# Optimization experiments

Measured on AMD Instinct MI355X. Metric: run time of the kernel, lower is better.

The kernel has to match this reference:

```python
import jax, jax.numpy as jnp
import numpy as np

N = 50000      # nodes
E = 800000     # edges (avg degree 16)
IN = 128       # in_size
OUT = 64       # out_size
H = 32         # hidden_size
WIDTH = 3      # width
SCALE = 0.05


def _laplacian(x, src, tgt, n):
    # normalized Laplacian action: out[t] = sum_{edges into t} (x[t] - x[s]) / deg(t)
    deg = jax.ops.segment_sum(jnp.ones((tgt.shape[0],), x.dtype), tgt, num_segments=n)
    fac = 1.0 / deg[tgt]                       # [E], deg>=1 for any target that appears
    msg = (x[tgt] - x[src]) * fac[:, None]     # [E, F]
    return jax.ops.segment_sum(msg, tgt, num_segments=n)


def _grouped_linear(x, Wg, bg):
    # Conv1d(kernel=1, groups=width) == per-group linear
    n = x.shape[0]
    xg = x.reshape(n, WIDTH, -1)               # [N, width, h_in]
    out = jnp.einsum('nwh,who->nwo', xg, Wg) + bg
    return out.reshape(n, -1)                  # [N, width*h_out]


def setup_inputs() -> dict:
    key = jax.random.key(0)
    ks = jax.random.split(key, 14)
    data = jax.random.normal(ks[0], (N, IN), jnp.float32)
    src = jax.random.randint(ks[1], (E,), 0, N)
    tgt = jnp.sort(jax.random.randint(ks[2], (E,), 0, N))
    # preprocess ConvSkip: Linear(in, hidden*width) + Linear(in, hidden*width)
    W_pre = jax.random.normal(ks[3], (IN, H * WIDTH), jnp.float32) * SCALE
    b_pre = jnp.zeros((H * WIDTH,), jnp.float32)
    T_pre = jax.random.normal(ks[4], (IN, H * WIDTH), jnp.float32) * SCALE
    bT_pre = jnp.zeros((H * WIDTH,), jnp.float32)
    # middle WideConvSkip (depth-2 = 1 block): grouped conv [width, H, H]
    W_blk = jax.random.normal(ks[5], (WIDTH, H, H), jnp.float32) * SCALE
    b_blk = jnp.zeros((WIDTH, H), jnp.float32)
    T_blk = jax.random.normal(ks[6], (IN, H * WIDTH), jnp.float32) * SCALE
    bT_blk = jnp.zeros((H * WIDTH,), jnp.float32)
    # postprocess WideConvSkip: grouped conv [width, H, OUT]
    W_post = jax.random.normal(ks[7], (WIDTH, H, OUT), jnp.float32) * SCALE
    b_post = jnp.zeros((WIDTH, OUT), jnp.float32)
    T_post = jax.random.normal(ks[8], (IN, OUT * WIDTH), jnp.float32) * SCALE
    bT_post = jnp.zeros((OUT * WIDTH,), jnp.float32)
    return {"data": data, "src": src, "tgt": tgt,
            "W_pre": W_pre, "b_pre": b_pre, "T_pre": T_pre, "bT_pre": bT_pre,
            "W_blk": W_blk, "b_blk": b_blk, "T_blk": T_blk, "bT_blk": bT_blk,
            "W_post": W_post, "b_post": b_post, "T_post": T_post, "bT_post": bT_post}


def reference(data, src, tgt, W_pre, b_pre, T_pre, bT_pre,
              W_blk, b_blk, T_blk, bT_blk,
              W_post, b_post, T_post, bT_post):
    n = data.shape[0]
    # preprocess ConvSkip: sigma(L f(x) + g(x))
    out = data @ W_pre + b_pre
    out = _laplacian(out, src, tgt, n)
    out = jax.nn.relu(out + data @ T_pre + bT_pre)       # [N, H*width]
    # middle WideConvSkip (depth - 2 = 1)
    h = _grouped_linear(out, W_blk, b_blk)
    h = _laplacian(h, src, tgt, n)
    out = jax.nn.relu(h + data @ T_blk + bT_blk)          # [N, H*width]
    # postprocess WideConvSkip
    h = _grouped_linear(out, W_post, b_post)
    h = _laplacian(h, src, tgt, n)
    out = jax.nn.relu(h + data @ T_post + bT_post)        # [N, OUT*width]
    # reshape(N, -1, width) then adaptive_avg_pool1d(., 1) == mean over width
    out = out.reshape(n, -1, WIDTH)
    return out.mean(axis=-1, keepdims=True)               # [N, OUT, 1]
```

## Files before the change

### kernel.cpp

```cpp
#include <hip/hip_runtime.h>
#include <cstdint>
#include <cstddef>

#define N_NODES 50000
#define E_EDGES 800000
#define IN_F    128
#define PCOLS   512

typedef unsigned short ushortT;
typedef unsigned int   uintT;
typedef __attribute__((ext_vector_type(8))) short s8v;
typedef __attribute__((ext_vector_type(4))) float f4v;
typedef __attribute__((ext_vector_type(2))) float f2v;

__device__ __forceinline__ float bflo(uintT u){ union{uintT i;float f;}c; c.i=u<<16; return c.f; }
__device__ __forceinline__ float bfhi(uintT u){ union{uintT i;float f;}c; c.i=u&0xFFFF0000u; return c.f; }
__device__ __forceinline__ ushortT f2bfu(float f){
    union{float f;uintT u;}c; c.f=f;
    uintT r = c.u + 0x7FFF + ((c.u>>16)&1);
    return (ushortT)(r>>16);
}
__device__ __forceinline__ uintT pack2(float a, float b){
    return (uintT)f2bfu(a) | ((uintT)f2bfu(b) << 16);
}

__global__ void prep1(const float* __restrict__ A,
                      const float* __restrict__ Wp,  const float* __restrict__ bp,
                      const float* __restrict__ Tp,  const float* __restrict__ bTp,
                      const float* __restrict__ Tb,  const float* __restrict__ bTb,
                      const float* __restrict__ Tpo, const float* __restrict__ bTpo,
                      const float* __restrict__ Wpost,
                      const int* __restrict__ tgt,
                      ushortT* __restrict__ Wb, float* __restrict__ bcat,
                      float2* __restrict__ Wp2,
                      ushortT* __restrict__ Ab, int* __restrict__ row_ptr)
{
    int gid = blockIdx.x * 256 + threadIdx.x;
    {
        size_t off = (size_t)gid * 8;
        float4 v0 = *(const float4*)(A + off);
        float4 v1 = *(const float4*)(A + off + 4);
        uint4 u;
        u.x = pack2(v0.x, v0.y); u.y = pack2(v0.z, v0.w);
        u.z = pack2(v1.x, v1.y); u.w = pack2(v1.z, v1.w);
        *(uint4*)(Ab + off) = u;
    }
    if (gid < IN_F * PCOLS) {
        int k = gid >> 9;
        int c = gid & 511;
        float v;
        if      (c < 96)  v = Wp [k*96  + c];
        else if (c < 192) v = Tp [k*96  + (c-96)];
        else if (c < 288) v = Tb [k*96  + (c-192)];
        else if (c < 480) v = Tpo[k*192 + (c-288)];
        else              v = 0.f;
        Wb[(size_t)c*IN_F + k] = f2bfu(v);
        if (k == 0) {
            float b;
            if      (c < 96)  b = bp  [c];
            else if (c < 192) b = bTp [c-96];
            else if (c < 288) b = bTb [c-192];
            else if (c < 480) b = bTpo[c-288];
            else              b = 0.f;
            bcat[c] = b;
        }
        if (gid < 3*16*64) {
            int w = gid >> 10, r = gid & 1023;
            int i2 = r >> 6, j = r & 63;
            Wp2[gid] = make_float2(Wpost[(w*32 + 2*i2)*64 + j],
                                   Wpost[(w*32 + 2*i2 + 1)*64 + j]);
        }
    }
    if (gid <= N_NODES) {
        int lo = 0, hi = E_EDGES;
        while (lo < hi) {
            int mid = (lo + hi) >> 1;
            if (tgt[mid] < gid) lo = mid + 1; else hi = mid;
        }
        row_ptr[gid] = lo;
    }
}

__global__ void build_srcp(const int* __restrict__ src, const int* __restrict__ row_ptr,
                           int* __restrict__ srcp,
                           ushortT* __restrict__ Y0b, ushortT* __restrict__ rb1,
                           ushortT* __restrict__ rb2)
{
    int gid = blockIdx.x * 256 + threadIdx.x;
    int t = gid >> 6, slot = gid & 63;
    int lo = row_ptr[t];
    int deg = row_ptr[t+1] - lo;
    int v = slot < deg ? src[lo + slot] : N_NODES;
    srcp[gid] = v * 192;
    if (gid < 96) {
        Y0b[(size_t)N_NODES*96 + gid] = 0;
        rb1[(size_t)N_NODES*96 + gid] = 0;
        rb2[(size_t)N_NODES*96 + gid] = 0;
    }
}

__global__ __launch_bounds__(256, 2) void gemm_mfma(const ushortT* __restrict__ Ab,
                                                    const ushortT* __restrict__ Wb,
                                                    const float* __restrict__ bcat,
                                                    float* __restrict__ P,
                                                    ushortT* __restrict__ Y0b, int M)
{
    __shared__ ushortT Asl[128][72];
    __shared__ ushortT Bsl[128][72];
    int tid = threadIdx.x;
    int nb = blockIdx.x * 128;
    int mb = blockIdx.y * 128;
    int wv = tid >> 6, lane = tid & 63;
    int wm = wv >> 1, wn = wv & 1;
    int cl = lane & 15, q = lane >> 4;

    f4v acc[4][4];
    #pragma unroll
    for (int i = 0; i < 4; ++i)
        #pragma unroll
        for (int j = 0; j < 4; ++j) acc[i][j] = (f4v)0.f;

    for (int kt = 0; kt < IN_F; kt += 64) {
        if (kt) __syncthreads();
        #pragma unroll
        for (int r = 0; r < 4; ++r) {
            int idx = tid + 256*r;
            int row = idx >> 3, qq = idx & 7;
            int gm = mb + row;
            uint4 v = make_uint4(0,0,0,0);
            if (gm < M) v = *(const uint4*)(Ab + (size_t)gm*IN_F + kt + qq*8);
            *(uint4*)(&Asl[row][qq*8]) = v;
        }
        #pragma unroll
        for (int r = 0; r < 4; ++r) {
            int idx = tid + 256*r;
            int row = idx >> 3, qq = idx & 7;
            uint4 v = *(const uint4*)(Wb + (size_t)(nb+row)*IN_F + kt + qq*8);
            *(uint4*)(&Bsl[row][qq*8]) = v;
        }
        __syncthreads();
        #pragma unroll
        for (int ks = 0; ks < 2; ++ks) {
            int ko = ks*32 + q*8;
            s8v af[4], bf[4];
            #pragma unroll
            for (int mt = 0; mt < 4; ++mt)
                af[mt] = *(const s8v*)(&Asl[wm*64 + mt*16 + cl][ko]);
            #pragma unroll
            for (int nt = 0; nt < 4; ++nt)
                bf[nt] = *(const s8v*)(&Bsl[wn*64 + nt*16 + cl][ko]);
            #pragma unroll
            for (int mt = 0; mt < 4; ++mt)
                #pragma unroll
                for (int nt = 0; nt < 4; ++nt)
                    acc[mt][nt] = __builtin_amdgcn_mfma_f32_16x16x32_bf16(af[mt], bf[nt], acc[mt][nt], 0, 0, 0);
        }
    }

    bool y0blk = (nb == 0) && (wn == 0);
    #pragma unroll
    for (int nt = 0; nt < 4; ++nt) {
        int gn = nb + wn*64 + nt*16 + cl;
        float bv = bcat[gn];
        bool doY = y0blk && (gn < 96);
        #pragma unroll
        for (int mt = 0; mt < 4; ++mt) {
            int gm0 = mb + wm*64 + mt*16 + q*4;
            #pragma unroll
            for (int r = 0; r < 4; ++r) {
                int gm = gm0 + r;
                if (gm < M) {
                    float val = acc[mt][nt][r] + bv;
                    P[(size_t)gm*PCOLS + gn] = val;
                    if (doY) Y0b[(size_t)gm*96 + gn] = f2bfu(val);
                }
            }
        }
    }
}

#define GATHER96(Xb, lo, deg, sv, pL, sx, sy)                                     \
    float sx, sy;                                                                 \
    {                                                                             \
        f2v c0={0.f,0.f}, c1={0.f,0.f}, c2={0.f,0.f}, c3={0.f,0.f};               \
        int dmax = deg < 64 ? deg : 64;                                           \
        _Pragma("unroll 1")                                                       \
        for (int w_ = 0; w_ < dmax; w_ += 16) {                                   \
            uintT u[16];                                                          \
            _Pragma("unroll")                                                     \
            for (int kk = 0; kk < 16; ++kk) {                                     \
                int off = __builtin_amdgcn_readlane(sv, w_ + kk);                 \
                const char* rp = (const char*)(Xb) + off;                         \
                u[kk] = *(const uintT*)(rp + 4*pL);                               \
            }                                                                     \
            _Pragma("unroll")                                                     \
            for (int kk = 0; kk < 16; ++kk) {                                     \
                f2v v_; v_.x = bflo(u[kk]); v_.y = bfhi(u[kk]);                   \
                switch (kk & 3) {                                                 \
                    case 0: c0 += v_; break;                                      \
                    case 1: c1 += v_; break;                                      \
                    case 2: c2 += v_; break;                                      \
                    default:c3 += v_; break;                                      \
                }                                                                 \
            }                                                                     \
        }                                                                         \
        if (deg > 64) {                                                           \
            _Pragma("unroll 1")                                                   \
            for (int j_ = lo + 64; j_ < lo + deg; ++j_) {                         \
                int off = src[j_] * 192;                                          \
                const char* rp = (const char*)(Xb) + off;                         \
                uintT u0 = *(const uintT*)(rp + 4*pL);                            \
                f2v v_; v_.x = bflo(u0); v_.y = bfhi(u0);                         \
                c0 += v_;                                                         \
            }                                                                     \
        }                                                                         \
        f2v cs_ = (c0 + c1) + (c2 + c3);                                          \
        sx = cs_.x; sy = cs_.y;                                                   \
    }

__global__ __launch_bounds__(256) void lap1(
    const ushortT* __restrict__ Xb,
    const float*   __restrict__ Pown,
    const float*   __restrict__ Z,
    const int* __restrict__ srcp, const int* __restrict__ src,
    const int* __restrict__ row_ptr,
    ushortT* __restrict__ rb1)
{
    int lane = threadIdx.x & 63;
    int t  = __builtin_amdgcn_readfirstlane((blockIdx.x << 2) + (threadIdx.x >> 6));
    int lo = __builtin_amdgcn_readfirstlane(row_ptr[t]);
    int deg = __builtin_amdgcn_readfirstlane(row_ptr[t+1]) - lo;
    int pL = lane < 48 ? lane : 0;
    int sv = srcp[t*64 + lane];
    float2 xr = *(const float2*)(Pown + (size_t)t*PCOLS + 2*pL);
    float2 zr = *(const float2*)(Z    + (size_t)t*PCOLS + 2*pL);

    GATHER96(Xb, lo, deg, sv, pL, sx, sy)

    float inv = deg > 0 ? 1.f/(float)deg : 0.f;
    float mf  = deg > 0 ? 1.f : 0.f;
    if (lane < 48) {
        float ox = fmaxf(mf*xr.x - sx*inv + zr.x, 0.f);
        float oy = fmaxf(mf*xr.y - sy*inv + zr.y, 0.f);
        *(uintT*)(rb1 + (size_t)t*96 + 2*pL) = pack2(ox, oy);
    }
}

__global__ __launch_bounds__(256) void lap2(
    const ushortT* __restrict__ Xb,
    const float*   __restrict__ Z,
    const int* __restrict__ srcp, const int* __restrict__ src,
    const int* __restrict__ row_ptr,
    const float* __restrict__ Wblk,
    ushortT* __restrict__ rb2)
{
    __shared__ float wS[3*32*32];
    int lane = threadIdx.x & 63;
    int t  = __builtin_amdgcn_readfirstlane((blockIdx.x << 2) + (threadIdx.x >> 6));
    int pL = lane < 48 ? lane : 0;
    int sv = srcp[t*64 + lane];
    int lo = __builtin_amdgcn_readfirstlane(row_ptr[t]);
    int deg = __builtin_amdgcn_readfirstlane(row_ptr[t+1]) - lo;
    uintT ux = *(const uintT*)(Xb + (size_t)t*96 + 2*pL);
    float2 zr = *(const float2*)(Z + (size_t)t*PCOLS + 2*pL);

    for (int i = threadIdx.x; i < 3072; i += 256) wS[i] = Wblk[i];
    __syncthreads();

    int w  = pL >> 4;
    int jj = pL & 15;
    const float2* wc = ((const float2*)wS) + (w*512 + jj);

    GATHER96(Xb, lo, deg, sv, pL, sx, sy)

    float inv = deg > 0 ? 1.f/(float)deg : 0.f;
    float mf  = deg > 0 ? 1.f : 0.f;
    float Lx = mf*bflo(ux) - sx*inv;
    float Ly = mf*bfhi(ux) - sy*inv;

    float accx = 0.f, accy = 0.f;
    #pragma unroll
    for (int d = 0; d < 16; ++d) {
        int sl = w*16 + d;
        float ax = __shfl(Lx, sl);
        float ay = __shfl(Ly, sl);
        float2 wa = wc[(2*d)*16];
        float2 wb = wc[(2*d+1)*16];
        accx = fmaf(ax, wa.x, accx); accx = fmaf(ay, wb.x, accx);
        accy = fmaf(ax, wa.y, accy); accy = fmaf(ay, wb.y, accy);
    }
    if (lane < 48) {
        float ox = fmaxf(accx + zr.x, 0.f);
        float oy = fmaxf(accy + zr.y, 0.f);
        *(uintT*)(rb2 + (size_t)t*96 + 2*pL) = pack2(ox, oy);
    }
}

__global__ __launch_bounds__(256) void lap3(
    const ushortT* __restrict__ Xb,
    const float*   __restrict__ Z,
    const int* __restrict__ srcp, const int* __restrict__ src,
    const int* __restrict__ row_ptr,
    const float2* __restrict__ Wp2,
    float* __restrict__ out)
{
    __shared__ float2 wS[3*16*64];
    __shared__ float  sm[4][96];
    int lane = threadIdx.x & 63;
    int wvw  = threadIdx.x >> 6;
    int t  = __builtin_amdgcn_readfirstlane((blockIdx.x << 2) + wvw);
    int pL = lane < 48 ? lane : 0;
    int sv = srcp[t*64 + lane];
    int lo = __builtin_amdgcn_readfirstlane(row_ptr[t]);
    int deg = __builtin_amdgcn_readfirstlane(row_ptr[t+1]) - lo;
    uintT ux = *(const uintT*)(Xb + (size_t)t*96 + 2*pL);
    float z0 = Z[(size_t)t*PCOLS + lane];
    float z1 = Z[(size_t)t*PCOLS + 64 + lane];
    float z2 = Z[(size_t)t*PCOLS + 128 + lane];

    for (int i = threadIdx.x; i < 3072; i += 256) wS[i] = Wp2[i];
    __syncthreads();

    const float2* wl = wS + lane;

    GATHER96(Xb, lo, deg, sv, pL, sx, sy)

    float inv = deg > 0 ? 1.f/(float)deg : 0.f;
    float mf  = deg > 0 ? 1.f : 0.f;
    float Lx = mf*bflo(ux) - sx*inv;
    float Ly = mf*bfhi(ux) - sy*inv;

    if (lane < 48) {
        sm[wvw][2*pL]     = Lx;
        sm[wvw][2*pL + 1] = Ly;
    }
    __builtin_amdgcn_wave_barrier();

    float a0 = 0.f, a1 = 0.f, a2 = 0.f;
    #pragma unroll
    for (int w2 = 0; w2 < 3; ++w2) {
        float acc = 0.f;
        #pragma unroll
        for (int i2 = 0; i2 < 16; ++i2) {
            float2 iv = *(const float2*)(&sm[wvw][w2*32 + 2*i2]);
            float2 p  = wl[(w2*16 + i2)*64];
            acc = fmaf(iv.x, p.x, acc);
            acc = fmaf(iv.y, p.y, acc);
        }
        if (w2 == 0) a0 = acc; else if (w2 == 1) a1 = acc; else a2 = acc;
    }
    float o0 = fmaxf(a0 + z0, 0.f);
    float o1 = fmaxf(a1 + z1, 0.f);
    float o2 = fmaxf(a2 + z2, 0.f);
    float r = 0.f;
    #pragma unroll
    for (int q = 0; q < 3; ++q) {
        int c = 3*lane + q;
        int sl = c & 63, wsel = c >> 6;
        float v0 = __shfl(o0, sl);
        float v1 = __shfl(o1, sl);
        float v2 = __shfl(o2, sl);
        r += (wsel == 0) ? v0 : ((wsel == 1) ? v1 : v2);
    }
    out[(size_t)t*64 + lane] = r * (1.0f/3.0f);
}

extern "C" void kernel_launch(void* const* d_in, const int* in_sizes, int n_in,
                              void* d_out, int out_size, void* d_ws, size_t ws_size,
                              hipStream_t stream)
{
    const float* data    = (const float*)d_in[0];
    const int*   src     = (const int*)  d_in[1];
    const int*   tgt     = (const int*)  d_in[2];
    const float* W_pre   = (const float*)d_in[3];
    const float* b_pre   = (const float*)d_in[4];
    const float* T_pre   = (const float*)d_in[5];
    const float* bT_pre  = (const float*)d_in[6];
    const float* W_blk   = (const float*)d_in[7];
    const float* b_blk   = (const float*)d_in[8];
    const float* T_blk   = (const float*)d_in[9];
    const float* bT_blk  = (const float*)d_in[10];
    const float* W_post  = (const float*)d_in[11];
    const float* b_post  = (const float*)d_in[12];
    const float* T_post  = (const float*)d_in[13];
    const float* bT_post = (const float*)d_in[14];
    float* out = (float*)d_out;

    float* ws = (float*)d_ws;
    float*   P       = ws;
    float*   bcat    = P + (size_t)N_NODES * PCOLS;
    float2*  Wp2     = (float2*)(bcat + 512);
    int*     row_ptr = (int*)(Wp2 + 3*16*64);
    int*     srcp    = row_ptr + 50008;
    ushortT* Y0b     = (ushortT*)(srcp + (size_t)N_NODES*64);
    ushortT* rb1     = Y0b + (size_t)(N_NODES+1) * 96;
    ushortT* rb2     = rb1 + (size_t)(N_NODES+1) * 96;
    ushortT* Ab      = rb2 + (size_t)(N_NODES+1) * 96;
    ushortT* Wb      = Ab  + (size_t)N_NODES * IN_F;

    prep1<<<(N_NODES*IN_F/8)/256, 256, 0, stream>>>(
        data, W_pre, b_pre, T_pre, bT_pre, T_blk, bT_blk, T_post, bT_post,
        W_post, tgt, Wb, bcat, Wp2, Ab, row_ptr);

    build_srcp<<<(N_NODES*64)/256, 256, 0, stream>>>(src, row_ptr, srcp, Y0b, rb1, rb2);

    dim3 gg(PCOLS/128, (N_NODES + 127)/128);
    gemm_mfma<<<gg, 256, 0, stream>>>(Ab, Wb, bcat, P, Y0b, N_NODES);

    lap1<<<N_NODES/4, 256, 0, stream>>>(Y0b, P, P + 96, srcp, src, row_ptr, rb1);
    lap2<<<N_NODES/4, 256, 0, stream>>>(rb1, P + 192, srcp, src, row_ptr, W_blk, rb2);
    lap3<<<N_NODES/4, 256, 0, stream>>>(rb2, P + 288, srcp, src, row_ptr, Wp2, out);
}
```

Before: 303.5 us.

## Store GEMM output in bf16, drop srcp precompute, loop nodes per block

The GEMM now writes its whole 512-column output as bf16 instead of fp32 plus a separate bf16 copy, roughly halving that write traffic and the later reads of the skip terms. The build_srcp kernel is removed; each Laplacian kernel loads its neighbour indices straight from src and scales them by the row stride, with the zero padding row moved into prep1. lap2 and lap3 now process four nodes per wave so each block stages its weights in shared memory once for sixteen nodes instead of four. The cost is bf16 rounding of the skip and Laplacian inputs, and the first layer gathers from rows with a wider 512-column stride.

```diff
diff --git a/kernel.cpp b/kernel.cpp
--- a/kernel.cpp
+++ b/kernel.cpp
@@ -33,7 +33,9 @@
                       const int* __restrict__ tgt,
                       ushortT* __restrict__ Wb, float* __restrict__ bcat,
                       float2* __restrict__ Wp2,
-                      ushortT* __restrict__ Ab, int* __restrict__ row_ptr)
+                      ushortT* __restrict__ Ab, int* __restrict__ row_ptr,
+                      ushortT* __restrict__ Pb, ushortT* __restrict__ rb1,
+                      ushortT* __restrict__ rb2)
 {
     int gid = blockIdx.x * 256 + threadIdx.x;
     {
@@ -71,6 +73,11 @@
                                    Wpost[(w*32 + 2*i2 + 1)*64 + j]);
         }
     }
+    if (gid < 96) {
+        Pb [(size_t)N_NODES*PCOLS + gid] = 0;
+        rb1[(size_t)N_NODES*96   + gid] = 0;
+        rb2[(size_t)N_NODES*96   + gid] = 0;
+    }
     if (gid <= N_NODES) {
         int lo = 0, hi = E_EDGES;
         while (lo < hi) {
@@ -81,29 +88,10 @@
     }
 }
 
-__global__ void build_srcp(const int* __restrict__ src, const int* __restrict__ row_ptr,
-                           int* __restrict__ srcp,
-                           ushortT* __restrict__ Y0b, ushortT* __restrict__ rb1,
-                           ushortT* __restrict__ rb2)
-{
-    int gid = blockIdx.x * 256 + threadIdx.x;
-    int t = gid >> 6, slot = gid & 63;
-    int lo = row_ptr[t];
-    int deg = row_ptr[t+1] - lo;
-    int v = slot < deg ? src[lo + slot] : N_NODES;
-    srcp[gid] = v * 192;
-    if (gid < 96) {
-        Y0b[(size_t)N_NODES*96 + gid] = 0;
-        rb1[(size_t)N_NODES*96 + gid] = 0;
-        rb2[(size_t)N_NODES*96 + gid] = 0;
-    }
-}
-
 __global__ __launch_bounds__(256, 2) void gemm_mfma(const ushortT* __restrict__ Ab,
                                                     const ushortT* __restrict__ Wb,
                                                     const float* __restrict__ bcat,
-                                                    float* __restrict__ P,
-                                                    ushortT* __restrict__ Y0b, int M)
+                                                    ushortT* __restrict__ Pb, int M)
 {
     __shared__ ushortT Asl[128][72];
     __shared__ ushortT Bsl[128][72];
@@ -157,29 +145,23 @@
         }
     }
 
-    bool y0blk = (nb == 0) && (wn == 0);
     #pragma unroll
     for (int nt = 0; nt < 4; ++nt) {
         int gn = nb + wn*64 + nt*16 + cl;
         float bv = bcat[gn];
-        bool doY = y0blk && (gn < 96);
         #pragma unroll
         for (int mt = 0; mt < 4; ++mt) {
             int gm0 = mb + wm*64 + mt*16 + q*4;
             #pragma unroll
             for (int r = 0; r < 4; ++r) {
                 int gm = gm0 + r;
-                if (gm < M) {
-                    float val = acc[mt][nt][r] + bv;
-                    P[(size_t)gm*PCOLS + gn] = val;
-                    if (doY) Y0b[(size_t)gm*96 + gn] = f2bfu(val);
-                }
+                if (gm < M) Pb[(size_t)gm*PCOLS + gn] = f2bfu(acc[mt][nt][r] + bv);
             }
         }
     }
 }
 
-#define GATHER96(Xb, lo, deg, sv, pL, sx, sy)                                     \
+#define GATHER96(Xb, lo, deg, sv, pL, STRB, sx, sy)                               \
     float sx, sy;                                                                 \
     {                                                                             \
         f2v c0={0.f,0.f}, c1={0.f,0.f}, c2={0.f,0.f}, c3={0.f,0.f};               \
@@ -207,7 +189,7 @@
         if (deg > 64) {                                                           \
             _Pragma("unroll 1")                                                   \
             for (int j_ = lo + 64; j_ < lo + deg; ++j_) {                         \
-                int off = src[j_] * 192;                                          \
+                int off = src[j_] * (STRB);                                       \
                 const char* rp = (const char*)(Xb) + off;                         \
                 uintT u0 = *(const uintT*)(rp + 4*pL);                            \
                 f2v v_; v_.x = bflo(u0); v_.y = bfhi(u0);                         \
@@ -218,12 +200,18 @@
         sx = cs_.x; sy = cs_.y;                                                   \
     }
 
+#define MAKE_SV(lo, deg, lane, STRB, sv)                                          \
+    int sv;                                                                       \
+    {                                                                             \
+        int e_ = (lo) + (lane);                                                   \
+        if (e_ > E_EDGES - 1) e_ = E_EDGES - 1;                                   \
+        int sn_ = src[e_];                                                        \
+        sv = ((lane) < (deg) ? sn_ : N_NODES) * (STRB);                           \
+    }
+
 __global__ __launch_bounds__(256) void lap1(
-    const ushortT* __restrict__ Xb,
-    const float*   __restrict__ Pown,
-    const float*   __restrict__ Z,
-    const int* __restrict__ srcp, const int* __restrict__ src,
-    const int* __restrict__ row_ptr,
+    const ushortT* __restrict__ Pb,
+    const int* __restrict__ src, const int* __restrict__ row_ptr,
     ushortT* __restrict__ rb1)
 {
     int lane = threadIdx.x & 63;
@@ -231,138 +219,145 @@
     int lo = __builtin_amdgcn_readfirstlane(row_ptr[t]);
     int deg = __builtin_amdgcn_readfirstlane(row_ptr[t+1]) - lo;
     int pL = lane < 48 ? lane : 0;
-    int sv = srcp[t*64 + lane];
-    float2 xr = *(const float2*)(Pown + (size_t)t*PCOLS + 2*pL);
-    float2 zr = *(const float2*)(Z    + (size_t)t*PCOLS + 2*pL);
-
-    GATHER96(Xb, lo, deg, sv, pL, sx, sy)
+    MAKE_SV(lo, deg, lane, 2*PCOLS, sv)
+    uintT ux = *(const uintT*)(Pb + (size_t)t*PCOLS + 2*pL);
+    uintT zu = *(const uintT*)(Pb + (size_t)t*PCOLS + 96 + 2*pL);
+
+    GATHER96(Pb, lo, deg, sv, pL, 2*PCOLS, sx, sy)
 
     float inv = deg > 0 ? 1.f/(float)deg : 0.f;
     float mf  = deg > 0 ? 1.f : 0.f;
     if (lane < 48) {
-        float ox = fmaxf(mf*xr.x - sx*inv + zr.x, 0.f);
-        float oy = fmaxf(mf*xr.y - sy*inv + zr.y, 0.f);
+        float ox = fmaxf(mf*bflo(ux) - sx*inv + bflo(zu), 0.f);
+        float oy = fmaxf(mf*bfhi(ux) - sy*inv + bfhi(zu), 0.f);
         *(uintT*)(rb1 + (size_t)t*96 + 2*pL) = pack2(ox, oy);
     }
 }
 
 __global__ __launch_bounds__(256) void lap2(
     const ushortT* __restrict__ Xb,
-    const float*   __restrict__ Z,
-    const int* __restrict__ srcp, const int* __restrict__ src,
-    const int* __restrict__ row_ptr,
+    const ushortT* __restrict__ Pb,
+    const int* __restrict__ src, const int* __restrict__ row_ptr,
     const float* __restrict__ Wblk,
     ushortT* __restrict__ rb2)
 {
     __shared__ float wS[3*32*32];
-    int lane = threadIdx.x & 63;
-    int t  = __builtin_amdgcn_readfirstlane((blockIdx.x << 2) + (threadIdx.x >> 6));
-    int pL = lane < 48 ? lane : 0;
-    int sv = srcp[t*64 + lane];
-    int lo = __builtin_amdgcn_readfirstlane(row_ptr[t]);
-    int deg = __builtin_amdgcn_readfirstlane(row_ptr[t+1]) - lo;
-    uintT ux = *(const uintT*)(Xb + (size_t)t*96 + 2*pL);
-    float2 zr = *(const float2*)(Z + (size_t)t*PCOLS + 2*pL);
-
     for (int i = threadIdx.x; i < 3072; i += 256) wS[i] = Wblk[i];
     __syncthreads();
 
+    int lane = threadIdx.x & 63;
+    int wvw  = threadIdx.x >> 6;
+    int pL = lane < 48 ? lane : 0;
     int w  = pL >> 4;
     int jj = pL & 15;
     const float2* wc = ((const float2*)wS) + (w*512 + jj);
 
-    GATHER96(Xb, lo, deg, sv, pL, sx, sy)
-
-    float inv = deg > 0 ? 1.f/(float)deg : 0.f;
-    float mf  = deg > 0 ? 1.f : 0.f;
-    float Lx = mf*bflo(ux) - sx*inv;
-    float Ly = mf*bfhi(ux) - sy*inv;
-
-    float accx = 0.f, accy = 0.f;
-    #pragma unroll
-    for (int d = 0; d < 16; ++d) {
-        int sl = w*16 + d;
-        float ax = __shfl(Lx, sl);
-        float ay = __shfl(Ly, sl);
-        float2 wa = wc[(2*d)*16];
-        float2 wb = wc[(2*d+1)*16];
-        accx = fmaf(ax, wa.x, accx); accx = fmaf(ay, wb.x, accx);
-        accy = fmaf(ax, wa.y, accy); accy = fmaf(ay, wb.y, accy);
-    }
-    if (lane < 48) {
-        float ox = fmaxf(accx + zr.x, 0.f);
-        float oy = fmaxf(accy + zr.y, 0.f);
-        *(uintT*)(rb2 + (size_t)t*96 + 2*pL) = pack2(ox, oy);
+    #pragma unroll 1
+    for (int it = 0; it < 4; ++it) {
+        int t  = __builtin_amdgcn_readfirstlane(blockIdx.x*16 + it*4 + wvw);
+        int lo = __builtin_amdgcn_readfirstlane(row_ptr[t]);
+        int deg = __builtin_amdgcn_readfirstlane(row_ptr[t+1]) - lo;
+        MAKE_SV(lo, deg, lane, 192, sv)
+        uintT ux = *(const uintT*)(Xb + (size_t)t*96 + 2*pL);
+        uintT zu = *(const uintT*)(Pb + (size_t)t*PCOLS + 192 + 2*pL);
+
+        GATHER96(Xb, lo, deg, sv, pL, 192, sx, sy)
+
+        float inv = deg > 0 ? 1.f/(float)deg : 0.f;
+        float mf  = deg > 0 ? 1.f : 0.f;
+        float Lx = mf*bflo(ux) - sx*inv;
+        float Ly = mf*bfhi(ux) - sy*inv;
+
+        float accx = 0.f, accy = 0.f;
+        #pragma unroll
+        for (int d = 0; d < 16; ++d) {
+            int sl = w*16 + d;
+            float ax = __shfl(Lx, sl);
+            float ay = __shfl(Ly, sl);
+            float2 wa = wc[(2*d)*16];
+            float2 wb = wc[(2*d+1)*16];
+            accx = fmaf(ax, wa.x, accx); accx = fmaf(ay, wb.x, accx);
+            accy = fmaf(ax, wa.y, accy); accy = fmaf(ay, wb.y, accy);
+        }
+        if (lane < 48) {
+            float ox = fmaxf(accx + bflo(zu), 0.f);
+            float oy = fmaxf(accy + bfhi(zu), 0.f);
+            *(uintT*)(rb2 + (size_t)t*96 + 2*pL) = pack2(ox, oy);
+        }
     }
 }
 
 __global__ __launch_bounds__(256) void lap3(
     const ushortT* __restrict__ Xb,
-    const float*   __restrict__ Z,
-    const int* __restrict__ srcp, const int* __restrict__ src,
-    const int* __restrict__ row_ptr,
+    const ushortT* __restrict__ Pb,
+    const int* __restrict__ src, const int* __restrict__ row_ptr,
     const float2* __restrict__ Wp2,
     float* __restrict__ out)
 {
     __shared__ float2 wS[3*16*64];
     __shared__ float  sm[4][96];
+    for (int i = threadIdx.x; i < 3072; i += 256) wS[i] = Wp2[i];
+    __syncthreads();
+
     int lane = threadIdx.x & 63;
     int wvw  = threadIdx.x >> 6;
-    int t  = __builtin_amdgcn_readfirstlane((blockIdx.x << 2) + wvw);
     int pL = lane < 48 ? lane : 0;
-    int sv = srcp[t*64 + lane];
-    int lo = __builtin_amdgcn_readfirstlane(row_ptr[t]);
-    int deg = __builtin_amdgcn_readfirstlane(row_ptr[t+1]) - lo;
-    uintT ux = *(const uintT*)(Xb + (size_t)t*96 + 2*pL);
-    float z0 = Z[(size_t)t*PCOLS + lane];
-    float z1 = Z[(size_t)t*PCOLS + 64 + lane];
-    float z2 = Z[(size_t)t*PCOLS + 128 + lane];
-
-    for (int i = threadIdx.x; i < 3072; i += 256) wS[i] = Wp2[i];
-    __syncthreads();
-
     const float2* wl = wS + lane;
 
-    GATHER96(Xb, lo, deg, sv, pL, sx, sy)
-
-    float inv = deg > 0 ? 1.f/(float)deg : 0.f;
-    float mf  = deg > 0 ? 1.f : 0.f;
-    float Lx = mf*bflo(ux) - sx*inv;
-    float Ly = mf*bfhi(ux) - sy*inv;
-
-    if (lane < 48) {
-        sm[wvw][2*pL]     = Lx;
-        sm[wvw][2*pL + 1] = Ly;
-    }
-    __builtin_amdgcn_wave_barrier();
-
-    float a0 = 0.f, a1 = 0.f, a2 = 0.f;
-    #pragma unroll
-    for (int w2 = 0; w2 < 3; ++w2) {
-        float acc = 0.f;
-        #pragma unroll
-        for (int i2 = 0; i2 < 16; ++i2) {
-            float2 iv = *(const float2*)(&sm[wvw][w2*32 + 2*i2]);
-            float2 p  = wl[(w2*16 + i2)*64];
-            acc = fmaf(iv.x, p.x, acc);
-            acc = fmaf(iv.y, p.y, acc);
-        }
-        if (w2 == 0) a0 = acc; else if (w2 == 1) a1 = acc; else a2 = acc;
-    }
-    float o0 = fmaxf(a0 + z0, 0.f);
-    float o1 = fmaxf(a1 + z1, 0.f);
-    float o2 = fmaxf(a2 + z2, 0.f);
-    float r = 0.f;
-    #pragma unroll
-    for (int q = 0; q < 3; ++q) {
-        int c = 3*lane + q;
-        int sl = c & 63, wsel = c >> 6;
-        float v0 = __shfl(o0, sl);
-        float v1 = __shfl(o1, sl);
-        float v2 = __shfl(o2, sl);
-        r += (wsel == 0) ? v0 : ((wsel == 1) ? v1 : v2);
-    }
-    out[(size_t)t*64 + lane] = r * (1.0f/3.0f);
+    #pragma unroll 1
+    for (int it = 0; it < 4; ++it) {
+        int t  = __builtin_amdgcn_readfirstlane(blockIdx.x*16 + it*4 + wvw);
+        int lo = __builtin_amdgcn_readfirstlane(row_ptr[t]);
+        int deg = __builtin_amdgcn_readfirstlane(row_ptr[t+1]) - lo;
+        MAKE_SV(lo, deg, lane, 192, sv)
+        uintT ux = *(const uintT*)(Xb + (size_t)t*96 + 2*pL);
+        float z0 = bflo((uintT)Pb[(size_t)t*PCOLS + 288 + lane]);
+        float z1 = bflo((uintT)Pb[(size_t)t*PCOLS + 352 + lane]);
+        float z2 = bflo((uintT)Pb[(size_t)t*PCOLS + 416 + lane]);
+
+        GATHER96(Xb, lo, deg, sv, pL, 192, sx, sy)
+
+        float inv = deg > 0 ? 1.f/(float)deg : 0.f;
+        float mf  = deg > 0 ? 1.f : 0.f;
+        float Lx = mf*bflo(ux) - sx*inv;
+        float Ly = mf*bfhi(ux) - sy*inv;
+
+        if (lane < 48) {
+            sm[wvw][2*pL]     = Lx;
+            sm[wvw][2*pL + 1] = Ly;
+        }
+        __builtin_amdgcn_wave_barrier();
+
+        float a0 = 0.f, a1 = 0.f, a2 = 0.f;
+        #pragma unroll
+        for (int w2 = 0; w2 < 3; ++w2) {
+            float acc = 0.f;
+            #pragma unroll
+            for (int i2 = 0; i2 < 16; ++i2) {
+                float2 iv = *(const float2*)(&sm[wvw][w2*32 + 2*i2]);
+                float2 p  = wl[(w2*16 + i2)*64];
+                acc = fmaf(iv.x, p.x, acc);
+                acc = fmaf(iv.y, p.y, acc);
+            }
+            if (w2 == 0) a0 = acc; else if (w2 == 1) a1 = acc; else a2 = acc;
+        }
+        __builtin_amdgcn_wave_barrier();
+
+        float o0 = fmaxf(a0 + z0, 0.f);
+        float o1 = fmaxf(a1 + z1, 0.f);
+        float o2 = fmaxf(a2 + z2, 0.f);
+        float r = 0.f;
+        #pragma unroll
+        for (int q = 0; q < 3; ++q) {
+            int c = 3*lane + q;
+            int sl = c & 63, wsel = c >> 6;
+            float v0 = __shfl(o0, sl);
+            float v1 = __shfl(o1, sl);
+            float v2 = __shfl(o2, sl);
+            r += (wsel == 0) ? v0 : ((wsel == 1) ? v1 : v2);
+        }
+        out[(size_t)t*64 + lane] = r * (1.0f/3.0f);
+    }
 }
 
 extern "C" void kernel_launch(void* const* d_in, const int* in_sizes, int n_in,
@@ -386,28 +381,24 @@
     const float* bT_post = (const float*)d_in[14];
     float* out = (float*)d_out;
 
-    float* ws = (float*)d_ws;
-    float*   P       = ws;
-    float*   bcat    = P + (size_t)N_NODES * PCOLS;
+    float*   ws      = (float*)d_ws;
+    float*   bcat    = ws;
     float2*  Wp2     = (float2*)(bcat + 512);
     int*     row_ptr = (int*)(Wp2 + 3*16*64);
-    int*     srcp    = row_ptr + 50008;
-    ushortT* Y0b     = (ushortT*)(srcp + (size_t)N_NODES*64);
-    ushortT* rb1     = Y0b + (size_t)(N_NODES+1) * 96;
+    ushortT* Pb      = (ushortT*)(row_ptr + 50008);
+    ushortT* rb1     = Pb  + (size_t)(N_NODES+1) * PCOLS;
     ushortT* rb2     = rb1 + (size_t)(N_NODES+1) * 96;
     ushortT* Ab      = rb2 + (size_t)(N_NODES+1) * 96;
     ushortT* Wb      = Ab  + (size_t)N_NODES * IN_F;
 
     prep1<<<(N_NODES*IN_F/8)/256, 256, 0, stream>>>(
         data, W_pre, b_pre, T_pre, bT_pre, T_blk, bT_blk, T_post, bT_post,
-        W_post, tgt, Wb, bcat, Wp2, Ab, row_ptr);
-
-    build_srcp<<<(N_NODES*64)/256, 256, 0, stream>>>(src, row_ptr, srcp, Y0b, rb1, rb2);
+        W_post, tgt, Wb, bcat, Wp2, Ab, row_ptr, Pb, rb1, rb2);
 
     dim3 gg(PCOLS/128, (N_NODES + 127)/128);
-    gemm_mfma<<<gg, 256, 0, stream>>>(Ab, Wb, bcat, P, Y0b, N_NODES);
-
-    lap1<<<N_NODES/4, 256, 0, stream>>>(Y0b, P, P + 96, srcp, src, row_ptr, rb1);
-    lap2<<<N_NODES/4, 256, 0, stream>>>(rb1, P + 192, srcp, src, row_ptr, W_blk, rb2);
-    lap3<<<N_NODES/4, 256, 0, stream>>>(rb2, P + 288, srcp, src, row_ptr, Wp2, out);
-}
+    gemm_mfma<<<gg, 256, 0, stream>>>(Ab, Wb, bcat, Pb, N_NODES);
+
+    lap1<<<N_NODES/4, 256, 0, stream>>>(Pb, src, row_ptr, rb1);
+    lap2<<<N_NODES/16, 256, 0, stream>>>(rb1, Pb, src, row_ptr, W_blk, rb2);
+    lap3<<<N_NODES/16, 256, 0, stream>>>(rb2, Pb, src, row_ptr, Wp2, out);
+}
```

New measurement: 285.8 us. 1.06x faster.
